# Performance work log

Hardware: AMD Instinct MI355X
Metric: run time of the kernel (lower is better)

The kernel has to match this reference:

```python
import jax, jax.numpy as jnp
import numpy as np

B, S, D, H = 4, 2048, 1024, 16
DH = D // H  # 64


def setup_inputs() -> dict:
    key = jax.random.key(0)
    ks = jax.random.split(key, 7)
    scale = 1.0 / np.sqrt(DH)
    return {
        "sequences": jax.random.normal(ks[0], (B, S, D), dtype=jnp.float32),
        # torch Linear weights: [out, in] per head -> stacked [H, DH, DH]
        "Wq": jax.random.uniform(ks[1], (H, DH, DH), jnp.float32, -scale, scale),
        "bq": jax.random.uniform(ks[2], (H, DH), jnp.float32, -scale, scale),
        "Wk": jax.random.uniform(ks[3], (H, DH, DH), jnp.float32, -scale, scale),
        "bk": jax.random.uniform(ks[4], (H, DH), jnp.float32, -scale, scale),
        "Wv": jax.random.uniform(ks[5], (H, DH, DH), jnp.float32, -scale, scale),
        "bv": jax.random.uniform(ks[6], (H, DH), jnp.float32, -scale, scale),
    }


def reference(sequences, Wq, bq, Wk, bk, Wv, bv):
    # split d into heads: [B, S, H, DH]
    x = sequences.reshape(B, S, H, DH)
    # per-head Linear: y = x @ W.T + b
    q = jnp.einsum("bshd,hed->bshe", x, Wq) + bq
    k = jnp.einsum("bshd,hed->bshe", x, Wk) + bk
    v = jnp.einsum("bshd,hed->bshe", x, Wv) + bv
    # scaled dot-product attention per head
    scores = jnp.einsum("bshd,bthd->bhst", q, k) / jnp.sqrt(jnp.float32(DH))
    attn = jax.nn.softmax(scores, axis=-1)
    out = jnp.einsum("bhst,bthd->bshd", attn, v)
    # hstack heads back to [B, S, D]
    return out.reshape(B, S, D)
```

## Files before the change

kernel.cpp:

```cpp
#include <hip/hip_runtime.h>
#include <hip/hip_bf16.h>


typedef unsigned short u16;
typedef unsigned int   u32;
typedef float  f32x4  __attribute__((ext_vector_type(4)));
typedef __bf16 bf16x4 __attribute__((ext_vector_type(4)));
typedef __bf16 bf16x8 __attribute__((ext_vector_type(8)));

#define NB 4
#define SS 2048
#define DDIM 1024
#define NH 16
#define DH 64

static __device__ __forceinline__ float fexp2(float x) {
#if __has_builtin(__builtin_amdgcn_exp2f)
    return __builtin_amdgcn_exp2f(x);
#else
    return exp2f(x);
#endif
}
static __device__ __forceinline__ bf16x4 cvt4(f32x4 v) {
    return __builtin_convertvector(v, bf16x4);
}
static __device__ __forceinline__ bf16x8 cvt8(f32x4 lo, f32x4 hi) {
    return __builtin_shufflevector(cvt4(lo), cvt4(hi), 0, 1, 2, 3, 4, 5, 6, 7);
}

#define WST 72

__global__ __launch_bounds__(256) void qkv_kernel(
        const float* __restrict__ x,
        const float* __restrict__ Wq, const float* __restrict__ bq,
        const float* __restrict__ Wk, const float* __restrict__ bk,
        const float* __restrict__ Wv, const float* __restrict__ bv,
        u16* __restrict__ Qw, u16* __restrict__ Kw, u16* __restrict__ Vt) {
    __shared__ __align__(16) u16 W_lds[3 * DH * WST];

    const int tid  = threadIdx.x;
    const int w    = tid >> 6;
    const int lane = tid & 63;
    const int quad = lane >> 4;
    const int c    = lane & 15;
    const int bid  = blockIdx.x;
    const int bh   = bid & 63;
    const int s0   = (bid >> 6) * 256;
    const int b    = bh >> 4, h = bh & 15;

    {
        const float* Wsrc[3] = {Wq + h*DH*DH, Wk + h*DH*DH, Wv + h*DH*DH};
        #pragma unroll
        for (int j = 0; j < 6; ++j) {
            const int m = j >> 1;
            const int chunk = ((j & 1) << 8) + tid;
            const float* src = Wsrc[m] + chunk * 8;
            f32x4 lo = *(const f32x4*)src;
            f32x4 hi = *(const f32x4*)(src + 4);
            const int row = chunk >> 3, c8 = chunk & 7;
            *(bf16x8*)&W_lds[(m*DH + row) * WST + c8*8] = cvt8(lo, hi);
        }
    }
    __syncthreads();

    bf16x8 wf[3][4][2];
    #pragma unroll
    for (int m = 0; m < 3; ++m)
        #pragma unroll
        for (int mt = 0; mt < 4; ++mt)
            #pragma unroll
            for (int kh = 0; kh < 2; ++kh)
                wf[m][mt][kh] = *(const bf16x8*)&W_lds[(m*DH + mt*16 + c) * WST + kh*32 + quad*8];

    f32x4 biasQK[2][4];
    float biasV[4];
    #pragma unroll
    for (int mt = 0; mt < 4; ++mt) {
        biasQK[0][mt] = *(const f32x4*)(bq + h*DH + mt*16 + quad*4);
        biasQK[1][mt] = *(const f32x4*)(bk + h*DH + mt*16 + quad*4);
        biasV[mt] = bv[h*DH + mt*16 + c];
    }

    const size_t qkbase = (size_t)bh * SS * DH;
    const size_t vtbase = (size_t)bh * DH * SS;

    #pragma unroll 1
    for (int g = 0; g < 4; ++g) {
        const int sb = s0 + w*64 + g*16;
        const float* xr = x + ((size_t)(b * SS + sb + c)) * DDIM + h * DH;
        bf16x8 xb[2];
        #pragma unroll
        for (int kh = 0; kh < 2; ++kh) {
            f32x4 lo = *(const f32x4*)(xr + kh*32 + quad*8);
            f32x4 hi = *(const f32x4*)(xr + kh*32 + quad*8 + 4);
            xb[kh] = cvt8(lo, hi);
        }

        const int srow = sb + c;
        const int tq = srow & 31;
        const int sK = (srow & ~31) | ((tq & 4) << 2) | ((tq >> 3) << 2) | (tq & 3);

        #pragma unroll
        for (int m = 0; m < 2; ++m) {
            const float scale = (m == 0) ? 0.18033688f : 1.0f;
            u16* base = (m == 0 ? Qw : Kw) + qkbase + (size_t)(m == 0 ? srow : sK) * DH;
            #pragma unroll
            for (int mt = 0; mt < 4; ++mt) {
                f32x4 acc = {0.f, 0.f, 0.f, 0.f};
                acc = __builtin_amdgcn_mfma_f32_16x16x32_bf16(wf[m][mt][0], xb[0], acc, 0, 0, 0);
                acc = __builtin_amdgcn_mfma_f32_16x16x32_bf16(wf[m][mt][1], xb[1], acc, 0, 0, 0);
                f32x4 v = (acc + biasQK[m][mt]) * scale;
                *(bf16x4*)(base + mt*16 + quad*4) = cvt4(v);
            }
        }
        #pragma unroll
        for (int nt = 0; nt < 4; ++nt) {
            f32x4 acc = {0.f, 0.f, 0.f, 0.f};
            acc = __builtin_amdgcn_mfma_f32_16x16x32_bf16(xb[0], wf[2][nt][0], acc, 0, 0, 0);
            acc = __builtin_amdgcn_mfma_f32_16x16x32_bf16(xb[1], wf[2][nt][1], acc, 0, 0, 0);
            f32x4 v = acc + biasV[nt];
            u16* dst = Vt + vtbase + (size_t)(nt*16 + c) * SS + sb + quad*4;
            *(bf16x4*)dst = cvt4(v);
        }
    }
}

#define KT 64
#define KST 72
#define VST 72

__global__ __launch_bounds__(256, 4) void attn_kernel(
        const u16* __restrict__ Qw, const u16* __restrict__ Kw,
        const u16* __restrict__ Vt, float* __restrict__ out) {
    __shared__ __align__(16) u16 K_lds[2][KT * KST];
    __shared__ __align__(16) u16 V_lds[2][DH * VST];

    const int tid  = threadIdx.x;
    const int w    = tid >> 6;
    const int lane = tid & 63;
    const int quad = lane >> 4;
    const int c    = lane & 15;
    const int bid  = blockIdx.x;
    const int bh   = bid & 63;
    const int q0   = (bid >> 6) * 128;
    const int qw   = q0 + w * 32;

    const u16* Qb = Qw + (size_t)bh * SS * DH;
    const u16* Kb = Kw + (size_t)bh * SS * DH;
    const u16* Vb = Vt + (size_t)bh * DH * SS;

    bf16x8 qf[2][2];
    #pragma unroll
    for (int qt = 0; qt < 2; ++qt) {
        const u16* qrow = Qb + (size_t)(qw + qt*16 + c) * DH;
        qf[qt][0] = *(const bf16x8*)(qrow + quad*8);
        qf[qt][1] = *(const bf16x8*)(qrow + 32 + quad*8);
    }

    f32x4 o[4][2];
    f32x4 lacc[2];
    #pragma unroll
    for (int qt = 0; qt < 2; ++qt) {
        lacc[qt] = (f32x4){0.f, 0.f, 0.f, 0.f};
        #pragma unroll
        for (int dt = 0; dt < 4; ++dt) o[dt][qt] = (f32x4){0.f, 0.f, 0.f, 0.f};
    }

    bf16x8 ones8;
    { union { u16 u[8]; bf16x8 v; } one;
      #pragma unroll
      for (int i = 0; i < 8; ++i) one.u[i] = 0x3F80;
      ones8 = one.v; }

    const int strow = tid >> 2;
    const int stcol = (tid & 3) * 16;
    const int kofs  = strow * KST + stcol;
    const int vofs  = strow * VST + stcol;

    uint4 kr0 = *(const uint4*)(Kb + (size_t)strow * DH + stcol);
    uint4 kr1 = *(const uint4*)(Kb + (size_t)strow * DH + stcol + 8);
    uint4 vr0 = *(const uint4*)(Vb + (size_t)strow * SS + stcol);
    uint4 vr1 = *(const uint4*)(Vb + (size_t)strow * SS + stcol + 8);

    #pragma unroll 1
    for (int t0 = 0; t0 < SS; t0 += KT) {
        const int bsel = (t0 >> 6) & 1;
        u16* Kl = K_lds[bsel];
        u16* Vl = V_lds[bsel];
        *(uint4*)&Kl[kofs]     = kr0;
        *(uint4*)&Kl[kofs + 8] = kr1;
        *(uint4*)&Vl[vofs]     = vr0;
        *(uint4*)&Vl[vofs + 8] = vr1;
        __syncthreads();
        int tn = t0 + KT; if (tn >= SS) tn = 0;
        kr0 = *(const uint4*)(Kb + (size_t)(tn + strow) * DH + stcol);
        kr1 = *(const uint4*)(Kb + (size_t)(tn + strow) * DH + stcol + 8);
        vr0 = *(const uint4*)(Vb + (size_t)strow * SS + tn + stcol);
        vr1 = *(const uint4*)(Vb + (size_t)strow * SS + tn + stcol + 8);

        #pragma unroll
        for (int g = 0; g < 2; ++g) {
            bf16x8 kfA0 = *(const bf16x8*)&Kl[(g*32 + c) * KST + quad*8];
            bf16x8 kfA1 = *(const bf16x8*)&Kl[(g*32 + c) * KST + 32 + quad*8];
            bf16x8 kfB0 = *(const bf16x8*)&Kl[(g*32 + 16 + c) * KST + quad*8];
            bf16x8 kfB1 = *(const bf16x8*)&Kl[(g*32 + 16 + c) * KST + 32 + quad*8];
            bf16x8 vf[4];
            #pragma unroll
            for (int dt = 0; dt < 4; ++dt)
                vf[dt] = *(const bf16x8*)&Vl[(dt*16 + c) * VST + g*32 + quad*8];

            #pragma unroll
            for (int qt = 0; qt < 2; ++qt) {
                f32x4 sA = {0.f,0.f,0.f,0.f}, sB = {0.f,0.f,0.f,0.f};
                sA = __builtin_amdgcn_mfma_f32_16x16x32_bf16(kfA0, qf[qt][0], sA, 0,0,0);
                sA = __builtin_amdgcn_mfma_f32_16x16x32_bf16(kfA1, qf[qt][1], sA, 0,0,0);
                sB = __builtin_amdgcn_mfma_f32_16x16x32_bf16(kfB0, qf[qt][0], sB, 0,0,0);
                sB = __builtin_amdgcn_mfma_f32_16x16x32_bf16(kfB1, qf[qt][1], sB, 0,0,0);
                f32x4 eA, eB;
                #pragma unroll
                for (int r = 0; r < 4; ++r) { eA[r] = fexp2(sA[r]); eB[r] = fexp2(sB[r]); }
                bf16x8 pf = cvt8(eA, eB);
                #pragma unroll
                for (int dt = 0; dt < 4; ++dt)
                    o[dt][qt] = __builtin_amdgcn_mfma_f32_16x16x32_bf16(vf[dt], pf, o[dt][qt], 0,0,0);
                lacc[qt] = __builtin_amdgcn_mfma_f32_16x16x32_bf16(ones8, pf, lacc[qt], 0,0,0);
            }
        }
    }

    const int b = bh >> 4, h = bh & 15;
    #pragma unroll
    for (int qt = 0; qt < 2; ++qt) {
        const float inv = 1.0f / lacc[qt][0];
        const int token = qw + qt*16 + c;
        float* orow = out + ((size_t)b * SS + token) * DDIM + h * DH;
        #pragma unroll
        for (int dt = 0; dt < 4; ++dt) {
            f32x4 vv = o[dt][qt] * inv;
            *(f32x4*)(orow + dt*16 + quad*4) = vv;
        }
    }
}

extern "C" void kernel_launch(void* const* d_in, const int* in_sizes, int n_in,
                              void* d_out, int out_size, void* d_ws, size_t ws_size,
                              hipStream_t stream) {
    const float* x  = (const float*)d_in[0];
    const float* Wq = (const float*)d_in[1];
    const float* bq = (const float*)d_in[2];
    const float* Wk = (const float*)d_in[3];
    const float* bk = (const float*)d_in[4];
    const float* Wv = (const float*)d_in[5];
    const float* bv = (const float*)d_in[6];

    u16* Qw = (u16*)d_ws;
    u16* Kw = Qw + (size_t)NB * NH * SS * DH;
    u16* Vt = Kw + (size_t)NB * NH * SS * DH;

    qkv_kernel<<<64 * (SS / 256), 256, 0, stream>>>(
        x, Wq, bq, Wk, bk, Wv, bv, Qw, Kw, Vt);
    attn_kernel<<<64 * (SS / 128), 256, 0, stream>>>(Qw, Kw, Vt, (float*)d_out);
}
```

Baseline: 181.9 us.

## Drop LDS staging in attention, load K/V fragments directly into registers

The attention kernel no longer stages K and V tiles through shared memory with a block barrier. Each wave now reads its MFMA fragments straight from global memory into two register buffers, loading the next half-tile while computing the current one. Blocks shrink to two waves of 64 queries each, which doubles per-wave K/V reuse but gives up cross-wave sharing and relies on the cache for it. The QKV projection kernel also moves to smaller 128-row blocks, launching twice as many of them.

```diff
diff --git a/kernel.cpp b/kernel.cpp
--- a/kernel.cpp
+++ b/kernel.cpp
@@ -30,7 +30,7 @@
 
 #define WST 72
 
-__global__ __launch_bounds__(256) void qkv_kernel(
+__global__ __launch_bounds__(256, 3) void qkv_kernel(
         const float* __restrict__ x,
         const float* __restrict__ Wq, const float* __restrict__ bq,
         const float* __restrict__ Wk, const float* __restrict__ bk,
@@ -45,7 +45,7 @@
     const int c    = lane & 15;
     const int bid  = blockIdx.x;
     const int bh   = bid & 63;
-    const int s0   = (bid >> 6) * 256;
+    const int s0   = (bid >> 6) * 128;
     const int b    = bh >> 4, h = bh & 15;
 
     {
@@ -85,8 +85,8 @@
     const size_t vtbase = (size_t)bh * DH * SS;
 
     #pragma unroll 1
-    for (int g = 0; g < 4; ++g) {
-        const int sb = s0 + w*64 + g*16;
+    for (int g = 0; g < 2; ++g) {
+        const int sb = s0 + w*32 + g*16;
         const float* xr = x + ((size_t)(b * SS + sb + c)) * DDIM + h * DH;
         bf16x8 xb[2];
         #pragma unroll
@@ -125,16 +125,39 @@
     }
 }
 
-#define KT 64
-#define KST 72
-#define VST 72
-
-__global__ __launch_bounds__(256, 4) void attn_kernel(
+
+#define ATTN_LOAD(kf, vf, t) do {                                              \
+        kf[0] = *(const bf16x8*)(Kc + (size_t)(t) * DH);                       \
+        kf[1] = *(const bf16x8*)(Kc + (size_t)(t) * DH + 32);                  \
+        kf[2] = *(const bf16x8*)(Kc + (size_t)((t) + 16) * DH);                \
+        kf[3] = *(const bf16x8*)(Kc + (size_t)((t) + 16) * DH + 32);           \
+        vf[0] = *(const bf16x8*)(Vc + (size_t)(t));                            \
+        vf[1] = *(const bf16x8*)(Vc + (size_t)16 * SS + (t));                  \
+        vf[2] = *(const bf16x8*)(Vc + (size_t)32 * SS + (t));                  \
+        vf[3] = *(const bf16x8*)(Vc + (size_t)48 * SS + (t));                  \
+    } while (0)
+
+#define ATTN_PHASE(kf, vf)                                                     \
+    _Pragma("unroll")                                                          \
+    for (int qt = 0; qt < 4; ++qt) {                                           \
+        f32x4 sA = {0.f,0.f,0.f,0.f}, sB = {0.f,0.f,0.f,0.f};                  \
+        sA = __builtin_amdgcn_mfma_f32_16x16x32_bf16(kf[0], qf[qt][0], sA, 0,0,0); \
+        sA = __builtin_amdgcn_mfma_f32_16x16x32_bf16(kf[1], qf[qt][1], sA, 0,0,0); \
+        sB = __builtin_amdgcn_mfma_f32_16x16x32_bf16(kf[2], qf[qt][0], sB, 0,0,0); \
+        sB = __builtin_amdgcn_mfma_f32_16x16x32_bf16(kf[3], qf[qt][1], sB, 0,0,0); \
+        f32x4 eA, eB;                                                          \
+        _Pragma("unroll")                                                      \
+        for (int r = 0; r < 4; ++r) { eA[r] = fexp2(sA[r]); eB[r] = fexp2(sB[r]); } \
+        bf16x8 pf = cvt8(eA, eB);                                              \
+        _Pragma("unroll")                                                      \
+        for (int dt = 0; dt < 4; ++dt)                                         \
+            o[dt][qt] = __builtin_amdgcn_mfma_f32_16x16x32_bf16(vf[dt], pf, o[dt][qt], 0,0,0); \
+        lacc[qt] = __builtin_amdgcn_mfma_f32_16x16x32_bf16(ones8, pf, lacc[qt], 0,0,0); \
+    }
+
+__global__ __launch_bounds__(128, 2) void attn_kernel(
         const u16* __restrict__ Qw, const u16* __restrict__ Kw,
         const u16* __restrict__ Vt, float* __restrict__ out) {
-    __shared__ __align__(16) u16 K_lds[2][KT * KST];
-    __shared__ __align__(16) u16 V_lds[2][DH * VST];
-
     const int tid  = threadIdx.x;
     const int w    = tid >> 6;
     const int lane = tid & 63;
@@ -143,24 +166,24 @@
     const int bid  = blockIdx.x;
     const int bh   = bid & 63;
     const int q0   = (bid >> 6) * 128;
-    const int qw   = q0 + w * 32;
+    const int qw   = q0 + w * 64;
 
     const u16* Qb = Qw + (size_t)bh * SS * DH;
-    const u16* Kb = Kw + (size_t)bh * SS * DH;
-    const u16* Vb = Vt + (size_t)bh * DH * SS;
-
-    bf16x8 qf[2][2];
-    #pragma unroll
-    for (int qt = 0; qt < 2; ++qt) {
+    const u16* Kc = Kw + (size_t)bh * SS * DH + (size_t)c * DH + quad * 8;
+    const u16* Vc = Vt + (size_t)bh * DH * SS + (size_t)c * SS + quad * 8;
+
+    bf16x8 qf[4][2];
+    #pragma unroll
+    for (int qt = 0; qt < 4; ++qt) {
         const u16* qrow = Qb + (size_t)(qw + qt*16 + c) * DH;
         qf[qt][0] = *(const bf16x8*)(qrow + quad*8);
         qf[qt][1] = *(const bf16x8*)(qrow + 32 + quad*8);
     }
 
-    f32x4 o[4][2];
-    f32x4 lacc[2];
-    #pragma unroll
-    for (int qt = 0; qt < 2; ++qt) {
+    f32x4 o[4][4];
+    f32x4 lacc[4];
+    #pragma unroll
+    for (int qt = 0; qt < 4; ++qt) {
         lacc[qt] = (f32x4){0.f, 0.f, 0.f, 0.f};
         #pragma unroll
         for (int dt = 0; dt < 4; ++dt) o[dt][qt] = (f32x4){0.f, 0.f, 0.f, 0.f};
@@ -172,65 +195,21 @@
       for (int i = 0; i < 8; ++i) one.u[i] = 0x3F80;
       ones8 = one.v; }
 
-    const int strow = tid >> 2;
-    const int stcol = (tid & 3) * 16;
-    const int kofs  = strow * KST + stcol;
-    const int vofs  = strow * VST + stcol;
-
-    uint4 kr0 = *(const uint4*)(Kb + (size_t)strow * DH + stcol);
-    uint4 kr1 = *(const uint4*)(Kb + (size_t)strow * DH + stcol + 8);
-    uint4 vr0 = *(const uint4*)(Vb + (size_t)strow * SS + stcol);
-    uint4 vr1 = *(const uint4*)(Vb + (size_t)strow * SS + stcol + 8);
-
+    bf16x8 kf0[4], vf0[4], kf1[4], vf1[4];
+
+    ATTN_LOAD(kf0, vf0, 0);
     #pragma unroll 1
-    for (int t0 = 0; t0 < SS; t0 += KT) {
-        const int bsel = (t0 >> 6) & 1;
-        u16* Kl = K_lds[bsel];
-        u16* Vl = V_lds[bsel];
-        *(uint4*)&Kl[kofs]     = kr0;
-        *(uint4*)&Kl[kofs + 8] = kr1;
-        *(uint4*)&Vl[vofs]     = vr0;
-        *(uint4*)&Vl[vofs + 8] = vr1;
-        __syncthreads();
-        int tn = t0 + KT; if (tn >= SS) tn = 0;
-        kr0 = *(const uint4*)(Kb + (size_t)(tn + strow) * DH + stcol);
-        kr1 = *(const uint4*)(Kb + (size_t)(tn + strow) * DH + stcol + 8);
-        vr0 = *(const uint4*)(Vb + (size_t)strow * SS + tn + stcol);
-        vr1 = *(const uint4*)(Vb + (size_t)strow * SS + tn + stcol + 8);
-
-        #pragma unroll
-        for (int g = 0; g < 2; ++g) {
-            bf16x8 kfA0 = *(const bf16x8*)&Kl[(g*32 + c) * KST + quad*8];
-            bf16x8 kfA1 = *(const bf16x8*)&Kl[(g*32 + c) * KST + 32 + quad*8];
-            bf16x8 kfB0 = *(const bf16x8*)&Kl[(g*32 + 16 + c) * KST + quad*8];
-            bf16x8 kfB1 = *(const bf16x8*)&Kl[(g*32 + 16 + c) * KST + 32 + quad*8];
-            bf16x8 vf[4];
-            #pragma unroll
-            for (int dt = 0; dt < 4; ++dt)
-                vf[dt] = *(const bf16x8*)&Vl[(dt*16 + c) * VST + g*32 + quad*8];
-
-            #pragma unroll
-            for (int qt = 0; qt < 2; ++qt) {
-                f32x4 sA = {0.f,0.f,0.f,0.f}, sB = {0.f,0.f,0.f,0.f};
-                sA = __builtin_amdgcn_mfma_f32_16x16x32_bf16(kfA0, qf[qt][0], sA, 0,0,0);
-                sA = __builtin_amdgcn_mfma_f32_16x16x32_bf16(kfA1, qf[qt][1], sA, 0,0,0);
-                sB = __builtin_amdgcn_mfma_f32_16x16x32_bf16(kfB0, qf[qt][0], sB, 0,0,0);
-                sB = __builtin_amdgcn_mfma_f32_16x16x32_bf16(kfB1, qf[qt][1], sB, 0,0,0);
-                f32x4 eA, eB;
-                #pragma unroll
-                for (int r = 0; r < 4; ++r) { eA[r] = fexp2(sA[r]); eB[r] = fexp2(sB[r]); }
-                bf16x8 pf = cvt8(eA, eB);
-                #pragma unroll
-                for (int dt = 0; dt < 4; ++dt)
-                    o[dt][qt] = __builtin_amdgcn_mfma_f32_16x16x32_bf16(vf[dt], pf, o[dt][qt], 0,0,0);
-                lacc[qt] = __builtin_amdgcn_mfma_f32_16x16x32_bf16(ones8, pf, lacc[qt], 0,0,0);
-            }
-        }
+    for (int t0 = 0; t0 < SS; t0 += 64) {
+        ATTN_LOAD(kf1, vf1, t0 + 32);
+        ATTN_PHASE(kf0, vf0);
+        const int tn = (t0 + 64 < SS) ? (t0 + 64) : 0;
+        ATTN_LOAD(kf0, vf0, tn);
+        ATTN_PHASE(kf1, vf1);
     }
 
     const int b = bh >> 4, h = bh & 15;
     #pragma unroll
-    for (int qt = 0; qt < 2; ++qt) {
+    for (int qt = 0; qt < 4; ++qt) {
         const float inv = 1.0f / lacc[qt][0];
         const int token = qw + qt*16 + c;
         float* orow = out + ((size_t)b * SS + token) * DDIM + h * DH;
@@ -257,7 +236,7 @@
     u16* Kw = Qw + (size_t)NB * NH * SS * DH;
     u16* Vt = Kw + (size_t)NB * NH * SS * DH;
 
-    qkv_kernel<<<64 * (SS / 256), 256, 0, stream>>>(
+    qkv_kernel<<<64 * (SS / 128), 256, 0, stream>>>(
         x, Wq, bq, Wk, bk, Wv, bv, Qw, Kw, Vt);
-    attn_kernel<<<64 * (SS / 128), 256, 0, stream>>>(Qw, Kw, Vt, (float*)d_out);
-}
+    attn_kernel<<<64 * (SS / 128), 128, 0, stream>>>(Qw, Kw, Vt, (float*)d_out);
+}
```

New measurement: 242.3 us. 33.2% more time.

## Load V fragments directly from global memory into registers, bypassing LDS staging

Applied to the files above, without the earlier changes.

V tiles are no longer staged through shared memory. Each lane now loads its transposed-V MFMA fragments straight from global memory (or L2), and the next half-tile is prefetched into registers while the current half is computed. This removes the V LDS writes and reads and halves LDS footprint, which may help occupancy. In exchange, every wave issues its own global loads for V, so the four waves fetch the same data redundantly, and the loads are 16-byte strided accesses across rows of length SS.

```diff
diff --git a/kernel.cpp b/kernel.cpp
--- a/kernel.cpp
+++ b/kernel.cpp
@@ -127,13 +127,35 @@
 
 #define KT 64
 #define KST 72
-#define VST 72
+
+#define ATTN_G(goff, vf)                                                       \
+    do {                                                                       \
+        bf16x8 kfA0 = *(const bf16x8*)&Kl[((goff) + c) * KST + quad*8];        \
+        bf16x8 kfA1 = *(const bf16x8*)&Kl[((goff) + c) * KST + 32 + quad*8];   \
+        bf16x8 kfB0 = *(const bf16x8*)&Kl[((goff) + 16 + c) * KST + quad*8];   \
+        bf16x8 kfB1 = *(const bf16x8*)&Kl[((goff) + 16 + c) * KST + 32 + quad*8]; \
+        _Pragma("unroll")                                                      \
+        for (int qt = 0; qt < 2; ++qt) {                                       \
+            f32x4 sA = {0.f,0.f,0.f,0.f}, sB = {0.f,0.f,0.f,0.f};              \
+            sA = __builtin_amdgcn_mfma_f32_16x16x32_bf16(kfA0, qf[qt][0], sA, 0,0,0); \
+            sA = __builtin_amdgcn_mfma_f32_16x16x32_bf16(kfA1, qf[qt][1], sA, 0,0,0); \
+            sB = __builtin_amdgcn_mfma_f32_16x16x32_bf16(kfB0, qf[qt][0], sB, 0,0,0); \
+            sB = __builtin_amdgcn_mfma_f32_16x16x32_bf16(kfB1, qf[qt][1], sB, 0,0,0); \
+            f32x4 eA, eB;                                                      \
+            _Pragma("unroll")                                                  \
+            for (int r = 0; r < 4; ++r) { eA[r] = fexp2(sA[r]); eB[r] = fexp2(sB[r]); } \
+            bf16x8 pf = cvt8(eA, eB);                                          \
+            _Pragma("unroll")                                                  \
+            for (int dt = 0; dt < 4; ++dt)                                     \
+                o[dt][qt] = __builtin_amdgcn_mfma_f32_16x16x32_bf16(vf[dt], pf, o[dt][qt], 0,0,0); \
+            lacc[qt] = __builtin_amdgcn_mfma_f32_16x16x32_bf16(ones8, pf, lacc[qt], 0,0,0); \
+        }                                                                      \
+    } while (0)
 
 __global__ __launch_bounds__(256, 4) void attn_kernel(
         const u16* __restrict__ Qw, const u16* __restrict__ Kw,
         const u16* __restrict__ Vt, float* __restrict__ out) {
     __shared__ __align__(16) u16 K_lds[2][KT * KST];
-    __shared__ __align__(16) u16 V_lds[2][DH * VST];
 
     const int tid  = threadIdx.x;
     const int w    = tid >> 6;
@@ -147,7 +169,7 @@
 
     const u16* Qb = Qw + (size_t)bh * SS * DH;
     const u16* Kb = Kw + (size_t)bh * SS * DH;
-    const u16* Vb = Vt + (size_t)bh * DH * SS;
+    const u16* Vc = Vt + (size_t)bh * DH * SS + (size_t)c * SS + quad * 8;
 
     bf16x8 qf[2][2];
     #pragma unroll
@@ -175,57 +197,35 @@
     const int strow = tid >> 2;
     const int stcol = (tid & 3) * 16;
     const int kofs  = strow * KST + stcol;
-    const int vofs  = strow * VST + stcol;
 
     uint4 kr0 = *(const uint4*)(Kb + (size_t)strow * DH + stcol);
     uint4 kr1 = *(const uint4*)(Kb + (size_t)strow * DH + stcol + 8);
-    uint4 vr0 = *(const uint4*)(Vb + (size_t)strow * SS + stcol);
-    uint4 vr1 = *(const uint4*)(Vb + (size_t)strow * SS + stcol + 8);
+
+    bf16x8 vfC[4], vfN[4];
+    #pragma unroll
+    for (int dt = 0; dt < 4; ++dt)
+        vfC[dt] = *(const bf16x8*)(Vc + (size_t)(dt*16) * SS);
 
     #pragma unroll 1
     for (int t0 = 0; t0 < SS; t0 += KT) {
         const int bsel = (t0 >> 6) & 1;
         u16* Kl = K_lds[bsel];
-        u16* Vl = V_lds[bsel];
         *(uint4*)&Kl[kofs]     = kr0;
         *(uint4*)&Kl[kofs + 8] = kr1;
-        *(uint4*)&Vl[vofs]     = vr0;
-        *(uint4*)&Vl[vofs + 8] = vr1;
         __syncthreads();
         int tn = t0 + KT; if (tn >= SS) tn = 0;
         kr0 = *(const uint4*)(Kb + (size_t)(tn + strow) * DH + stcol);
         kr1 = *(const uint4*)(Kb + (size_t)(tn + strow) * DH + stcol + 8);
-        vr0 = *(const uint4*)(Vb + (size_t)strow * SS + tn + stcol);
-        vr1 = *(const uint4*)(Vb + (size_t)strow * SS + tn + stcol + 8);
-
-        #pragma unroll
-        for (int g = 0; g < 2; ++g) {
-            bf16x8 kfA0 = *(const bf16x8*)&Kl[(g*32 + c) * KST + quad*8];
-            bf16x8 kfA1 = *(const bf16x8*)&Kl[(g*32 + c) * KST + 32 + quad*8];
-            bf16x8 kfB0 = *(const bf16x8*)&Kl[(g*32 + 16 + c) * KST + quad*8];
-            bf16x8 kfB1 = *(const bf16x8*)&Kl[(g*32 + 16 + c) * KST + 32 + quad*8];
-            bf16x8 vf[4];
-            #pragma unroll
-            for (int dt = 0; dt < 4; ++dt)
-                vf[dt] = *(const bf16x8*)&Vl[(dt*16 + c) * VST + g*32 + quad*8];
-
-            #pragma unroll
-            for (int qt = 0; qt < 2; ++qt) {
-                f32x4 sA = {0.f,0.f,0.f,0.f}, sB = {0.f,0.f,0.f,0.f};
-                sA = __builtin_amdgcn_mfma_f32_16x16x32_bf16(kfA0, qf[qt][0], sA, 0,0,0);
-                sA = __builtin_amdgcn_mfma_f32_16x16x32_bf16(kfA1, qf[qt][1], sA, 0,0,0);
-                sB = __builtin_amdgcn_mfma_f32_16x16x32_bf16(kfB0, qf[qt][0], sB, 0,0,0);
-                sB = __builtin_amdgcn_mfma_f32_16x16x32_bf16(kfB1, qf[qt][1], sB, 0,0,0);
-                f32x4 eA, eB;
-                #pragma unroll
-                for (int r = 0; r < 4; ++r) { eA[r] = fexp2(sA[r]); eB[r] = fexp2(sB[r]); }
-                bf16x8 pf = cvt8(eA, eB);
-                #pragma unroll
-                for (int dt = 0; dt < 4; ++dt)
-                    o[dt][qt] = __builtin_amdgcn_mfma_f32_16x16x32_bf16(vf[dt], pf, o[dt][qt], 0,0,0);
-                lacc[qt] = __builtin_amdgcn_mfma_f32_16x16x32_bf16(ones8, pf, lacc[qt], 0,0,0);
-            }
-        }
+
+        #pragma unroll
+        for (int dt = 0; dt < 4; ++dt)
+            vfN[dt] = *(const bf16x8*)(Vc + (size_t)(dt*16) * SS + t0 + 32);
+        ATTN_G(0, vfC);
+
+        #pragma unroll
+        for (int dt = 0; dt < 4; ++dt)
+            vfC[dt] = *(const bf16x8*)(Vc + (size_t)(dt*16) * SS + tn);
+        ATTN_G(32, vfN);
     }
 
     const int b = bh >> 4, h = bh & 15;
```

Result: slower. 250.7 us (+37.9%).

## Switch attention inner loop to 32x32x16 MFMA tiles with register row sums

Applied to the files above, without the earlier changes.

Replaces the 16x16x32 MFMA tiling in the attention kernel with 32x32x16 MFMAs, so each wave handles a 32-query tile with larger accumulators. K is permuted differently during projection to match the new P fragment layout. The softmax denominator is accumulated with scalar adds plus a cross-half shuffle instead of an extra ones-matrix MFMA. It also adds s_setprio around the compute section and lowers the launch-bounds occupancy hint from 4 to 2 to make room for the larger register footprint.

```diff
diff --git a/kernel.cpp b/kernel.cpp
--- a/kernel.cpp
+++ b/kernel.cpp
@@ -4,9 +4,10 @@
 
 typedef unsigned short u16;
 typedef unsigned int   u32;
-typedef float  f32x4  __attribute__((ext_vector_type(4)));
-typedef __bf16 bf16x4 __attribute__((ext_vector_type(4)));
-typedef __bf16 bf16x8 __attribute__((ext_vector_type(8)));
+typedef float  f32x4   __attribute__((ext_vector_type(4)));
+typedef float  f32x16  __attribute__((ext_vector_type(16)));
+typedef __bf16 bf16x4  __attribute__((ext_vector_type(4)));
+typedef __bf16 bf16x8  __attribute__((ext_vector_type(8)));
 
 #define NB 4
 #define SS 2048
@@ -98,7 +99,10 @@
 
         const int srow = sb + c;
         const int tq = srow & 31;
-        const int sK = (srow & ~31) | ((tq & 4) << 2) | ((tq >> 3) << 2) | (tq & 3);
+        const int sK = (srow & ~31) | (tq & 3)
+                     | (((tq >> 3) & 1) << 2)
+                     | (((tq >> 2) & 1) << 3)
+                     | (((tq >> 4) & 1) << 4);
 
         #pragma unroll
         for (int m = 0; m < 2; ++m) {
@@ -129,7 +133,39 @@
 #define KST 72
 #define VST 72
 
-__global__ __launch_bounds__(256, 4) void attn_kernel(
+#define Z16 {0.f,0.f,0.f,0.f,0.f,0.f,0.f,0.f,0.f,0.f,0.f,0.f,0.f,0.f,0.f,0.f}
+
+#define GROUP(g) do {                                                          \
+        bf16x8 ka0 = *(const bf16x8*)&Kl[((g)*32 + l31) * KST +  0 + hi*8];    \
+        bf16x8 ka1 = *(const bf16x8*)&Kl[((g)*32 + l31) * KST + 16 + hi*8];    \
+        bf16x8 ka2 = *(const bf16x8*)&Kl[((g)*32 + l31) * KST + 32 + hi*8];    \
+        bf16x8 ka3 = *(const bf16x8*)&Kl[((g)*32 + l31) * KST + 48 + hi*8];    \
+        bf16x8 vf00 = *(const bf16x8*)&Vl[( 0 + l31) * VST + (g)*32 +  0 + hi*8]; \
+        bf16x8 vf01 = *(const bf16x8*)&Vl[( 0 + l31) * VST + (g)*32 + 16 + hi*8]; \
+        bf16x8 vf10 = *(const bf16x8*)&Vl[(32 + l31) * VST + (g)*32 +  0 + hi*8]; \
+        bf16x8 vf11 = *(const bf16x8*)&Vl[(32 + l31) * VST + (g)*32 + 16 + hi*8]; \
+        __builtin_amdgcn_s_setprio(1);                                         \
+        f32x16 s = Z16;                                                        \
+        s = __builtin_amdgcn_mfma_f32_32x32x16_bf16(ka0, qf[0], s, 0,0,0);     \
+        s = __builtin_amdgcn_mfma_f32_32x32x16_bf16(ka1, qf[1], s, 0,0,0);     \
+        s = __builtin_amdgcn_mfma_f32_32x32x16_bf16(ka2, qf[2], s, 0,0,0);     \
+        s = __builtin_amdgcn_mfma_f32_32x32x16_bf16(ka3, qf[3], s, 0,0,0);     \
+        _Pragma("unroll")                                                      \
+        for (int r = 0; r < 16; ++r) s[r] = fexp2(s[r]);                       \
+        lp += (((s[0]+s[1])+(s[2]+s[3])) + ((s[4]+s[5])+(s[6]+s[7])))          \
+            + (((s[8]+s[9])+(s[10]+s[11])) + ((s[12]+s[13])+(s[14]+s[15])));   \
+        bf16x8 pf0 = cvt8((f32x4){s[0],s[1],s[2],s[3]},                        \
+                          (f32x4){s[4],s[5],s[6],s[7]});                       \
+        bf16x8 pf1 = cvt8((f32x4){s[8],s[9],s[10],s[11]},                      \
+                          (f32x4){s[12],s[13],s[14],s[15]});                   \
+        o0 = __builtin_amdgcn_mfma_f32_32x32x16_bf16(vf00, pf0, o0, 0,0,0);    \
+        o0 = __builtin_amdgcn_mfma_f32_32x32x16_bf16(vf01, pf1, o0, 0,0,0);    \
+        o1 = __builtin_amdgcn_mfma_f32_32x32x16_bf16(vf10, pf0, o1, 0,0,0);    \
+        o1 = __builtin_amdgcn_mfma_f32_32x32x16_bf16(vf11, pf1, o1, 0,0,0);    \
+        __builtin_amdgcn_s_setprio(0);                                         \
+    } while (0)
+
+__global__ __launch_bounds__(256, 2) void attn_kernel(
         const u16* __restrict__ Qw, const u16* __restrict__ Kw,
         const u16* __restrict__ Vt, float* __restrict__ out) {
     __shared__ __align__(16) u16 K_lds[2][KT * KST];
@@ -138,8 +174,8 @@
     const int tid  = threadIdx.x;
     const int w    = tid >> 6;
     const int lane = tid & 63;
-    const int quad = lane >> 4;
-    const int c    = lane & 15;
+    const int l31  = lane & 31;
+    const int hi   = lane >> 5;
     const int bid  = blockIdx.x;
     const int bh   = bid & 63;
     const int q0   = (bid >> 6) * 128;
@@ -149,28 +185,16 @@
     const u16* Kb = Kw + (size_t)bh * SS * DH;
     const u16* Vb = Vt + (size_t)bh * DH * SS;
 
-    bf16x8 qf[2][2];
-    #pragma unroll
-    for (int qt = 0; qt < 2; ++qt) {
-        const u16* qrow = Qb + (size_t)(qw + qt*16 + c) * DH;
-        qf[qt][0] = *(const bf16x8*)(qrow + quad*8);
-        qf[qt][1] = *(const bf16x8*)(qrow + 32 + quad*8);
-    }
-
-    f32x4 o[4][2];
-    f32x4 lacc[2];
-    #pragma unroll
-    for (int qt = 0; qt < 2; ++qt) {
-        lacc[qt] = (f32x4){0.f, 0.f, 0.f, 0.f};
-        #pragma unroll
-        for (int dt = 0; dt < 4; ++dt) o[dt][qt] = (f32x4){0.f, 0.f, 0.f, 0.f};
-    }
-
-    bf16x8 ones8;
-    { union { u16 u[8]; bf16x8 v; } one;
-      #pragma unroll
-      for (int i = 0; i < 8; ++i) one.u[i] = 0x3F80;
-      ones8 = one.v; }
+    bf16x8 qf[4];
+    {
+        const u16* qrow = Qb + (size_t)(qw + l31) * DH;
+        #pragma unroll
+        for (int m = 0; m < 4; ++m)
+            qf[m] = *(const bf16x8*)(qrow + m*16 + hi*8);
+    }
+
+    f32x16 o0 = Z16, o1 = Z16;
+    float lp = 0.f;
 
     const int strow = tid >> 2;
     const int stcol = (tid & 3) * 16;
@@ -198,47 +222,23 @@
         vr0 = *(const uint4*)(Vb + (size_t)strow * SS + tn + stcol);
         vr1 = *(const uint4*)(Vb + (size_t)strow * SS + tn + stcol + 8);
 
-        #pragma unroll
-        for (int g = 0; g < 2; ++g) {
-            bf16x8 kfA0 = *(const bf16x8*)&Kl[(g*32 + c) * KST + quad*8];
-            bf16x8 kfA1 = *(const bf16x8*)&Kl[(g*32 + c) * KST + 32 + quad*8];
-            bf16x8 kfB0 = *(const bf16x8*)&Kl[(g*32 + 16 + c) * KST + quad*8];
-            bf16x8 kfB1 = *(const bf16x8*)&Kl[(g*32 + 16 + c) * KST + 32 + quad*8];
-            bf16x8 vf[4];
-            #pragma unroll
-            for (int dt = 0; dt < 4; ++dt)
-                vf[dt] = *(const bf16x8*)&Vl[(dt*16 + c) * VST + g*32 + quad*8];
-
-            #pragma unroll
-            for (int qt = 0; qt < 2; ++qt) {
-                f32x4 sA = {0.f,0.f,0.f,0.f}, sB = {0.f,0.f,0.f,0.f};
-                sA = __builtin_amdgcn_mfma_f32_16x16x32_bf16(kfA0, qf[qt][0], sA, 0,0,0);
-                sA = __builtin_amdgcn_mfma_f32_16x16x32_bf16(kfA1, qf[qt][1], sA, 0,0,0);
-                sB = __builtin_amdgcn_mfma_f32_16x16x32_bf16(kfB0, qf[qt][0], sB, 0,0,0);
-                sB = __builtin_amdgcn_mfma_f32_16x16x32_bf16(kfB1, qf[qt][1], sB, 0,0,0);
-                f32x4 eA, eB;
-                #pragma unroll
-                for (int r = 0; r < 4; ++r) { eA[r] = fexp2(sA[r]); eB[r] = fexp2(sB[r]); }
-                bf16x8 pf = cvt8(eA, eB);
-                #pragma unroll
-                for (int dt = 0; dt < 4; ++dt)
-                    o[dt][qt] = __builtin_amdgcn_mfma_f32_16x16x32_bf16(vf[dt], pf, o[dt][qt], 0,0,0);
-                lacc[qt] = __builtin_amdgcn_mfma_f32_16x16x32_bf16(ones8, pf, lacc[qt], 0,0,0);
-            }
-        }
+        GROUP(0);
+        GROUP(1);
     }
 
     const int b = bh >> 4, h = bh & 15;
+    const float lw = lp + __shfl_xor(lp, 32, 64);
+    const float inv = 1.0f / lw;
+    const int token = qw + l31;
+    float* orow = out + ((size_t)b * SS + token) * DDIM + h * DH;
     #pragma unroll
-    for (int qt = 0; qt < 2; ++qt) {
-        const float inv = 1.0f / lacc[qt][0];
-        const int token = qw + qt*16 + c;
-        float* orow = out + ((size_t)b * SS + token) * DDIM + h * DH;
-        #pragma unroll
-        for (int dt = 0; dt < 4; ++dt) {
-            f32x4 vv = o[dt][qt] * inv;
-            *(f32x4*)(orow + dt*16 + quad*4) = vv;
-        }
+    for (int rq = 0; rq < 4; ++rq) {
+        f32x4 v0 = {o0[4*rq+0], o0[4*rq+1], o0[4*rq+2], o0[4*rq+3]};
+        f32x4 v1 = {o1[4*rq+0], o1[4*rq+1], o1[4*rq+2], o1[4*rq+3]};
+        v0 = v0 * inv;
+        v1 = v1 * inv;
+        *(f32x4*)(orow +      8*rq + 4*hi) = v0;
+        *(f32x4*)(orow + 32 + 8*rq + 4*hi) = v1;
     }
 }
 
```

Result: slower. 186.0 us (+2.3%).
